# Optimization experiments

Measured on AMD Instinct MI355X. Metric: run time of the kernel, lower is better.

## Reference

```python
import jax, jax.numpy as jnp
import numpy as np

B, S, D = 16, 4096, 128
LN_EPS = 1e-5
REC_EPS = 1e-8


def setup_inputs() -> dict:
    key = jax.random.key(0)
    k1, k2, k3, k4 = jax.random.split(key, 4)
    return {
        "C": jax.random.normal(k1, (B, S, D), dtype=jnp.float32),
        "V": jax.random.normal(k2, (B, S, D), dtype=jnp.float32),
        "W": jax.random.normal(k3, (B, S, D), dtype=jnp.float32),
        "encoder_context": jax.random.normal(k4, (B, D), dtype=jnp.float32),
        "time_modulation": jnp.full((1, 1, D), 0.5, dtype=jnp.float32),
        "context_modulation": jnp.full((1, D), 0.5, dtype=jnp.float32),
        "ln_weight": jnp.ones((D,), dtype=jnp.float32),
        "ln_bias": jnp.zeros((D,), dtype=jnp.float32),
    }


def reference(C, V, W, encoder_context, time_modulation, context_modulation, ln_weight, ln_bias):
    b_, s_, d_ = C.shape
    tm = time_modulation[0, 0]  # [D]
    # context gate is time-invariant: compute once
    ctx_add = jax.nn.sigmoid(encoder_context * context_modulation) * encoder_context  # [B,D]

    def step(carry, xs):
        a, bst = carry  # a: [B,1], bst: [B,D]
        c_t, v_t, w_t = xs  # each [B,D]
        decay = jax.nn.sigmoid(w_t * tm)  # [B,D]
        ec = jnp.exp(c_t)  # [B,D]
        a = decay.mean(axis=1, keepdims=True) * a + ec.sum(axis=1, keepdims=True)
        bst = decay * bst + ec * v_t + ctx_add
        out_t = bst / (a + REC_EPS)
        return (a, bst), out_t

    a0 = jnp.zeros((b_, 1), dtype=C.dtype)
    b0 = jnp.zeros((b_, d_), dtype=C.dtype)
    xs = (jnp.swapaxes(C, 0, 1), jnp.swapaxes(V, 0, 1), jnp.swapaxes(W, 0, 1))  # [S,B,D]
    _, ys = jax.lax.scan(step, (a0, b0), xs)  # ys: [S,B,D]
    res = jnp.swapaxes(ys, 0, 1)  # [B,S,D]

    mu = jnp.mean(res, axis=-1, keepdims=True)
    var = jnp.var(res, axis=-1, keepdims=True)
    normed = (res - mu) * jax.lax.rsqrt(var + LN_EPS)
    return normed * ln_weight + ln_bias
```

## Files before the change

### kernel.cpp

```cpp
#include <hip/hip_runtime.h>

#define BB   16
#define SS   4096
#define DD   128
#define NCH  512
#define TT   (SS / NCH)
#define WPB  4
#define NTHR 256
#define NWAVE (BB * NCH)

#define LN_EPS  1e-5f
#define REC_EPS 1e-8f

__device__ __forceinline__ float fast_rcp(float x) { return __builtin_amdgcn_rcpf(x); }
__device__ __forceinline__ float sigm(float x) { return fast_rcp(1.0f + __expf(-x)); }

template<int CTRL>
__device__ __forceinline__ float dpp_mov0(float x) {
    return __int_as_float(
        __builtin_amdgcn_update_dpp(0, __float_as_int(x), CTRL, 0xF, 0xF, true));
}

__device__ __forceinline__ void wave_red2(float& a, float& b) {
    a += dpp_mov0<0x111>(a); b += dpp_mov0<0x111>(b);
    a += dpp_mov0<0x112>(a); b += dpp_mov0<0x112>(b);
    a += dpp_mov0<0x114>(a); b += dpp_mov0<0x114>(b);
    a += dpp_mov0<0x118>(a); b += dpp_mov0<0x118>(b);
    a += dpp_mov0<0x142>(a); b += dpp_mov0<0x142>(b);
    a += dpp_mov0<0x143>(a); b += dpp_mov0<0x143>(b);
    a = __int_as_float(__builtin_amdgcn_readlane(__float_as_int(a), 63));
    b = __int_as_float(__builtin_amdgcn_readlane(__float_as_int(b), 63));
}

typedef const __attribute__((address_space(1))) unsigned int gas_u32;
typedef __attribute__((address_space(3))) unsigned int las_u32;
__device__ __forceinline__ void gload_lds16(const void* g, void* l) {
    __builtin_amdgcn_global_load_lds((gas_u32*)g, (las_u32*)l, 16, 0, 0);
}
#define VM_WAIT() asm volatile("s_waitcnt vmcnt(0)" ::: "memory")

__global__ __launch_bounds__(NTHR, 3) void pass1_kernel(
    const float* __restrict__ C, const float* __restrict__ V, const float* __restrict__ W,
    const float* __restrict__ enc, const float* __restrict__ tmod, const float* __restrict__ cmod,
    float2* __restrict__ PQ,
    float2* __restrict__ PaQa)
{
    __shared__ float lds[WPB][3][TT * DD];

    const int wv   = threadIdx.x >> 6;
    const int lane = threadIdx.x & 63;
    const int gc   = blockIdx.x * WPB + wv;
    const int b    = gc >> 9;
    const int ch   = gc & (NCH - 1);
    const int d2   = lane << 1;

    const int t0 = ch * TT;
    const size_t chunk = ((size_t)b * SS + t0) * DD;
    const char* Cc = (const char*)(C + chunk);
    const char* Wc = (const char*)(W + chunk);
    const char* Vc = (const char*)(V + chunk);

#pragma unroll
    for (int i = 0; i < 4; ++i) {
        const size_t bo = (size_t)i * 1024 + (size_t)lane * 16;
        gload_lds16(Cc + bo, &lds[wv][0][i * 256]);
        gload_lds16(Wc + bo, &lds[wv][1][i * 256]);
        gload_lds16(Vc + bo, &lds[wv][2][i * 256]);
    }

    const float2 tm = *(const float2*)(tmod + d2);
    const float2 cm = *(const float2*)(cmod + d2);
    const float2 ec = *(const float2*)(enc + b * DD + d2);

    VM_WAIT();

    float2 ctx;
    ctx.x = sigm(ec.x * cm.x) * ec.x;
    ctx.y = sigm(ec.y * cm.y) * ec.y;

    float2 P = make_float2(1.f, 1.f);
    float2 Q = make_float2(0.f, 0.f);
    float sdp[TT], sep[TT];

#pragma unroll
    for (int t = 0; t < TT; ++t) {
        const float2 cv = *(const float2*)&lds[wv][0][t * DD + d2];
        const float2 wl = *(const float2*)&lds[wv][1][t * DD + d2];
        const float2 vl = *(const float2*)&lds[wv][2][t * DD + d2];

        float2 dec, e2, T2;
        dec.x = sigm(wl.x * tm.x); dec.y = sigm(wl.y * tm.y);
        e2.x = __expf(cv.x); e2.y = __expf(cv.y);
        T2.x = e2.x * vl.x + ctx.x;
        T2.y = e2.y * vl.y + ctx.y;

        Q.x = dec.x * Q.x + T2.x;
        Q.y = dec.y * Q.y + T2.y;
        P.x *= dec.x; P.y *= dec.y;

        sdp[t] = dec.x + dec.y;
        sep[t] = e2.x + e2.y;
    }

#pragma unroll
    for (int t = 0; t < TT; ++t) wave_red2(sdp[t], sep[t]);

    float pa = 1.f, qa = 0.f;
#pragma unroll
    for (int t = 0; t < TT; ++t) {
        const float mt = sdp[t] * (1.0f / DD);
        pa *= mt;
        qa = mt * qa + sep[t];
    }

    float4 pq4;
    pq4.x = P.x; pq4.y = Q.x; pq4.z = P.y; pq4.w = Q.y;
    *(float4*)(PQ + (size_t)gc * DD + d2) = pq4;
    if (lane == 0) PaQa[gc] = make_float2(pa, qa);
}

__global__ __launch_bounds__(256, 4) void pass2_kernel(
    const float2* __restrict__ PQ, const float2* __restrict__ PaQa,
    float* __restrict__ bst0,
    float* __restrict__ a0)
{
    const int wv   = threadIdx.x >> 6;
    const int lane = threadIdx.x & 63;
    const int wid  = blockIdx.x * 4 + wv;

    if (wid < BB * DD) {
        const int b = wid >> 7;
        const int d = wid & (DD - 1);
        const int ch0 = lane * 8;
        const size_t base = ((size_t)b * NCH + ch0) * DD + d;

        float2 A[8];
#pragma unroll
        for (int i = 0; i < 8; ++i) A[i] = PQ[base + (size_t)i * DD];

        float p = 1.f, q = 0.f;
#pragma unroll
        for (int i = 0; i < 8; ++i) { q = A[i].x * q + A[i].y; p = A[i].x * p; }

#pragma unroll
        for (int dl = 1; dl < 64; dl <<= 1) {
            float ps = __shfl_up(p, dl);
            float qs = __shfl_up(q, dl);
            ps = (lane >= dl) ? ps : 1.f;
            qs = (lane >= dl) ? qs : 0.f;
            q = p * qs + q;
            p = p * ps;
        }

        float x = __shfl_up(q, 1);
        x = (lane >= 1) ? x : 0.f;

#pragma unroll
        for (int i = 0; i < 8; ++i) {
            bst0[base + (size_t)i * DD] = x;
            x = A[i].x * x + A[i].y;
        }
    } else if (wid < BB * DD + BB) {
        const int b = wid - BB * DD;
        const int ch0 = lane * 8;

        float2 A[8];
#pragma unroll
        for (int i = 0; i < 8; ++i) A[i] = PaQa[b * NCH + ch0 + i];

        float p = 1.f, q = 0.f;
#pragma unroll
        for (int i = 0; i < 8; ++i) { q = A[i].x * q + A[i].y; p = A[i].x * p; }

#pragma unroll
        for (int dl = 1; dl < 64; dl <<= 1) {
            float ps = __shfl_up(p, dl);
            float qs = __shfl_up(q, dl);
            ps = (lane >= dl) ? ps : 1.f;
            qs = (lane >= dl) ? qs : 0.f;
            q = p * qs + q;
            p = p * ps;
        }

        float x = __shfl_up(q, 1);
        x = (lane >= 1) ? x : 0.f;
#pragma unroll
        for (int i = 0; i < 8; ++i) {
            a0[b * NCH + ch0 + i] = x;
            x = A[i].x * x + A[i].y;
        }
    }
}

__global__ __launch_bounds__(NTHR, 3) void pass3_kernel(
    const float* __restrict__ C, const float* __restrict__ V, const float* __restrict__ W,
    const float* __restrict__ enc, const float* __restrict__ tmod, const float* __restrict__ cmod,
    const float* __restrict__ lnw, const float* __restrict__ lnb,
    const float* __restrict__ bst0, const float* __restrict__ a0,
    float* __restrict__ out)
{
    __shared__ float lds[WPB][3][TT * DD];

    const int wv   = threadIdx.x >> 6;
    const int lane = threadIdx.x & 63;
    const int gc   = blockIdx.x * WPB + wv;
    const int b    = gc >> 9;
    const int ch   = gc & (NCH - 1);
    const int d2   = lane << 1;

    const int t0 = ch * TT;
    const size_t chunk = ((size_t)b * SS + t0) * DD;
    const char* Cc = (const char*)(C + chunk);
    const char* Wc = (const char*)(W + chunk);
    const char* Vc = (const char*)(V + chunk);
    float2* Op = (float2*)(out + chunk + d2);

#pragma unroll
    for (int i = 0; i < 4; ++i) {
        const size_t bo = (size_t)i * 1024 + (size_t)lane * 16;
        gload_lds16(Cc + bo, &lds[wv][0][i * 256]);
        gload_lds16(Wc + bo, &lds[wv][1][i * 256]);
        gload_lds16(Vc + bo, &lds[wv][2][i * 256]);
    }

    const float2 tm = *(const float2*)(tmod + d2);
    const float2 cm = *(const float2*)(cmod + d2);
    const float2 ec = *(const float2*)(enc + b * DD + d2);
    const float2 gw = *(const float2*)(lnw + d2);
    const float2 gb = *(const float2*)(lnb + d2);
    float2 bst = *(const float2*)(bst0 + (size_t)gc * DD + d2);
    const float a_in = a0[gc];

    VM_WAIT();

    float2 ctx;
    ctx.x = sigm(ec.x * cm.x) * ec.x;
    ctx.y = sigm(ec.y * cm.y) * ec.y;

    float sdp[TT], sep[TT];
#pragma unroll
    for (int t = 0; t < TT; ++t) {
        const float2 cv = *(const float2*)&lds[wv][0][t * DD + d2];
        const float2 wl = *(const float2*)&lds[wv][1][t * DD + d2];
        sdp[t] = sigm(wl.x * tm.x) + sigm(wl.y * tm.y);
        sep[t] = __expf(cv.x) + __expf(cv.y);
    }
#pragma unroll
    for (int t = 0; t < TT; ++t) wave_red2(sdp[t], sep[t]);

    float a = a_in;
    float2 o[TT];
    float s1p[TT], s2p[TT];
#pragma unroll
    for (int t = 0; t < TT; ++t) {
        const float2 cv = *(const float2*)&lds[wv][0][t * DD + d2];
        const float2 wl = *(const float2*)&lds[wv][1][t * DD + d2];
        const float2 vl = *(const float2*)&lds[wv][2][t * DD + d2];

        float2 dec, e2, T2;
        dec.x = sigm(wl.x * tm.x); dec.y = sigm(wl.y * tm.y);
        e2.x = __expf(cv.x); e2.y = __expf(cv.y);
        T2.x = e2.x * vl.x + ctx.x;
        T2.y = e2.y * vl.y + ctx.y;

        const float mt = sdp[t] * (1.0f / DD);
        a = mt * a + sep[t];
        bst.x = dec.x * bst.x + T2.x;
        bst.y = dec.y * bst.y + T2.y;

        const float inva = fast_rcp(a + REC_EPS);
        o[t].x = bst.x * inva; o[t].y = bst.y * inva;
        s1p[t] = o[t].x + o[t].y;
        s2p[t] = o[t].x * o[t].x + o[t].y * o[t].y;
    }

#pragma unroll
    for (int t = 0; t < TT; ++t) wave_red2(s1p[t], s2p[t]);

#pragma unroll
    for (int t = 0; t < TT; ++t) {
        const float mu  = s1p[t] * (1.0f / DD);
        const float var = s2p[t] * (1.0f / DD) - mu * mu;
        const float rs  = rsqrtf(var + LN_EPS);
        float2 r;
        r.x = (o[t].x - mu) * rs * gw.x + gb.x;
        r.y = (o[t].y - mu) * rs * gw.y + gb.y;
        Op[t * (DD / 2)] = r;
    }
}

extern "C" void kernel_launch(void* const* d_in, const int* in_sizes, int n_in,
                              void* d_out, int out_size, void* d_ws, size_t ws_size,
                              hipStream_t stream)
{
    const float* C    = (const float*)d_in[0];
    const float* V    = (const float*)d_in[1];
    const float* W    = (const float*)d_in[2];
    const float* enc  = (const float*)d_in[3];
    const float* tmod = (const float*)d_in[4];
    const float* cmod = (const float*)d_in[5];
    const float* lnw  = (const float*)d_in[6];
    const float* lnb  = (const float*)d_in[7];
    float* out = (float*)d_out;

    float2* PQ   = (float2*)d_ws;
    float2* PaQa = PQ + (size_t)NWAVE * DD;
    float*  bst0 = (float*)(PaQa + NWAVE);
    float*  a0   = bst0 + (size_t)NWAVE * DD;

    const int nblk = NWAVE / WPB;
    pass1_kernel<<<nblk, NTHR, 0, stream>>>(C, V, W, enc, tmod, cmod, PQ, PaQa);
    pass2_kernel<<<(BB * DD + BB) / 4, 256, 0, stream>>>(PQ, PaQa, bst0, a0);
    pass3_kernel<<<nblk, NTHR, 0, stream>>>(C, V, W, enc, tmod, cmod, lnw, lnb,
                                            bst0, a0, out);
}
```

Baseline: 167.7 us.

## Process eight chunks per wave with double-buffered LDS prefetch in passes 1 and 3

Passes 1 and 3 now have each wave walk eight consecutive time chunks instead of one. C, W and V tiles are streamed into a two-slot LDS ring with global_load_lds, using explicit vmcnt waits so the next chunk's loads overlap the current chunk's compute. Blocks shrink to two waves and the grid shrinks eightfold, which cuts the number of resident waves per CU. Latency hiding now depends on the software pipeline rather than on wave-level parallelism.

Result: slower. 179.8 us (+7.2%).

```diff
diff --git a/kernel.cpp b/kernel.cpp
--- a/kernel.cpp
+++ b/kernel.cpp
@@ -5,9 +5,10 @@
 #define DD   128
 #define NCH  512
 #define TT   (SS / NCH)
-#define WPB  4
-#define NTHR 256
 #define NWAVE (BB * NCH)
+#define KCH  8
+#define P13_WPB 2
+#define P13_NBLK (NWAVE / KCH / P13_WPB)
 
 #define LN_EPS  1e-5f
 #define REC_EPS 1e-8f
@@ -37,92 +38,113 @@
 __device__ __forceinline__ void gload_lds16(const void* g, void* l) {
     __builtin_amdgcn_global_load_lds((gas_u32*)g, (las_u32*)l, 16, 0, 0);
 }
-#define VM_WAIT() asm volatile("s_waitcnt vmcnt(0)" ::: "memory")
-
-__global__ __launch_bounds__(NTHR, 3) void pass1_kernel(
+
+#define VMWAIT(n) asm volatile("s_waitcnt vmcnt(" #n ")" ::: "memory")
+#define LGKWAIT() asm volatile("s_waitcnt lgkmcnt(0)" ::: "memory")
+
+__global__ __launch_bounds__(128, 1) void pass1_kernel(
     const float* __restrict__ C, const float* __restrict__ V, const float* __restrict__ W,
     const float* __restrict__ enc, const float* __restrict__ tmod, const float* __restrict__ cmod,
     float2* __restrict__ PQ,
     float2* __restrict__ PaQa)
 {
-    __shared__ float lds[WPB][3][TT * DD];
+    __shared__ __align__(16) float lds[P13_WPB][2][3][TT * DD];
 
     const int wv   = threadIdx.x >> 6;
     const int lane = threadIdx.x & 63;
-    const int gc   = blockIdx.x * WPB + wv;
-    const int b    = gc >> 9;
-    const int ch   = gc & (NCH - 1);
+    const int wid  = blockIdx.x * P13_WPB + wv;
+    const int gc0  = wid * KCH;
+    const int b    = gc0 >> 9;
+    const int ch0  = gc0 & (NCH - 1);
     const int d2   = lane << 1;
 
-    const int t0 = ch * TT;
-    const size_t chunk = ((size_t)b * SS + t0) * DD;
-    const char* Cc = (const char*)(C + chunk);
-    const char* Wc = (const char*)(W + chunk);
-    const char* Vc = (const char*)(V + chunk);
-
-#pragma unroll
-    for (int i = 0; i < 4; ++i) {
-        const size_t bo = (size_t)i * 1024 + (size_t)lane * 16;
-        gload_lds16(Cc + bo, &lds[wv][0][i * 256]);
-        gload_lds16(Wc + bo, &lds[wv][1][i * 256]);
-        gload_lds16(Vc + bo, &lds[wv][2][i * 256]);
-    }
+    const size_t chunk0 = ((size_t)b * SS + ch0 * TT) * DD;
+    const char* Cc = (const char*)(C + chunk0);
+    const char* Wc = (const char*)(W + chunk0);
+    const char* Vc = (const char*)(V + chunk0);
+
+#define P1_ISSUE(k) do { \
+    LGKWAIT(); \
+    const char* Cb_ = Cc + (size_t)(k) * 4096 + (size_t)lane * 16; \
+    const char* Wb_ = Wc + (size_t)(k) * 4096 + (size_t)lane * 16; \
+    const char* Vb_ = Vc + (size_t)(k) * 4096 + (size_t)lane * 16; \
+    _Pragma("unroll") \
+    for (int i = 0; i < 4; ++i) { \
+        gload_lds16(Cb_ + i * 1024, &lds[wv][(k) & 1][0][i * 256]); \
+        gload_lds16(Wb_ + i * 1024, &lds[wv][(k) & 1][1][i * 256]); \
+        gload_lds16(Vb_ + i * 1024, &lds[wv][(k) & 1][2][i * 256]); \
+    } \
+} while (0)
+
+    P1_ISSUE(0);
+    P1_ISSUE(1);
 
     const float2 tm = *(const float2*)(tmod + d2);
     const float2 cm = *(const float2*)(cmod + d2);
     const float2 ec = *(const float2*)(enc + b * DD + d2);
-
-    VM_WAIT();
-
     float2 ctx;
     ctx.x = sigm(ec.x * cm.x) * ec.x;
     ctx.y = sigm(ec.y * cm.y) * ec.y;
 
-    float2 P = make_float2(1.f, 1.f);
-    float2 Q = make_float2(0.f, 0.f);
-    float sdp[TT], sep[TT];
-
-#pragma unroll
-    for (int t = 0; t < TT; ++t) {
-        const float2 cv = *(const float2*)&lds[wv][0][t * DD + d2];
-        const float2 wl = *(const float2*)&lds[wv][1][t * DD + d2];
-        const float2 vl = *(const float2*)&lds[wv][2][t * DD + d2];
-
-        float2 dec, e2, T2;
-        dec.x = sigm(wl.x * tm.x); dec.y = sigm(wl.y * tm.y);
-        e2.x = __expf(cv.x); e2.y = __expf(cv.y);
-        T2.x = e2.x * vl.x + ctx.x;
-        T2.y = e2.y * vl.y + ctx.y;
-
-        Q.x = dec.x * Q.x + T2.x;
-        Q.y = dec.y * Q.y + T2.y;
-        P.x *= dec.x; P.y *= dec.y;
-
-        sdp[t] = dec.x + dec.y;
-        sep[t] = e2.x + e2.y;
+    float2 Pr[KCH], Qr[KCH];
+    float paR[KCH], qaR[KCH];
+
+#define P1_CH(k) do { \
+    float2 P = make_float2(1.f, 1.f), Q = make_float2(0.f, 0.f); \
+    float sdp[TT], sep[TT]; \
+    _Pragma("unroll") \
+    for (int t = 0; t < TT; ++t) { \
+        const float2 cv = *(const float2*)&lds[wv][(k) & 1][0][t * DD + d2]; \
+        const float2 wl = *(const float2*)&lds[wv][(k) & 1][1][t * DD + d2]; \
+        const float2 vl = *(const float2*)&lds[wv][(k) & 1][2][t * DD + d2]; \
+        float2 dec, e2, T2; \
+        dec.x = sigm(wl.x * tm.x); dec.y = sigm(wl.y * tm.y); \
+        e2.x = __expf(cv.x); e2.y = __expf(cv.y); \
+        T2.x = e2.x * vl.x + ctx.x; \
+        T2.y = e2.y * vl.y + ctx.y; \
+        Q.x = dec.x * Q.x + T2.x; \
+        Q.y = dec.y * Q.y + T2.y; \
+        P.x *= dec.x; P.y *= dec.y; \
+        sdp[t] = dec.x + dec.y; sep[t] = e2.x + e2.y; \
+    } \
+    _Pragma("unroll") \
+    for (int t = 0; t < TT; ++t) wave_red2(sdp[t], sep[t]); \
+    float pa = 1.f, qa = 0.f; \
+    _Pragma("unroll") \
+    for (int t = 0; t < TT; ++t) { \
+        const float mt = sdp[t] * (1.0f / DD); \
+        pa *= mt; qa = mt * qa + sep[t]; \
+    } \
+    Pr[k] = P; Qr[k] = Q; paR[k] = pa; qaR[k] = qa; \
+} while (0)
+
+    VMWAIT(12); P1_CH(0); P1_ISSUE(2);
+    VMWAIT(12); P1_CH(1); P1_ISSUE(3);
+    VMWAIT(12); P1_CH(2); P1_ISSUE(4);
+    VMWAIT(12); P1_CH(3); P1_ISSUE(5);
+    VMWAIT(12); P1_CH(4); P1_ISSUE(6);
+    VMWAIT(12); P1_CH(5); P1_ISSUE(7);
+    VMWAIT(12); P1_CH(6);
+    VMWAIT(0);  P1_CH(7);
+
+#undef P1_ISSUE
+#undef P1_CH
+
+#pragma unroll
+    for (int k = 0; k < KCH; ++k) {
+        float4 pq4;
+        pq4.x = Pr[k].x; pq4.y = Qr[k].x; pq4.z = Pr[k].y; pq4.w = Qr[k].y;
+        *(float4*)(PQ + (size_t)(gc0 + k) * DD + d2) = pq4;
     }
-
-#pragma unroll
-    for (int t = 0; t < TT; ++t) wave_red2(sdp[t], sep[t]);
-
-    float pa = 1.f, qa = 0.f;
-#pragma unroll
-    for (int t = 0; t < TT; ++t) {
-        const float mt = sdp[t] * (1.0f / DD);
-        pa *= mt;
-        qa = mt * qa + sep[t];
+    if (lane == 0) {
+#pragma unroll
+        for (int k = 0; k < KCH; ++k) PaQa[gc0 + k] = make_float2(paR[k], qaR[k]);
     }
-
-    float4 pq4;
-    pq4.x = P.x; pq4.y = Q.x; pq4.z = P.y; pq4.w = Q.y;
-    *(float4*)(PQ + (size_t)gc * DD + d2) = pq4;
-    if (lane == 0) PaQa[gc] = make_float2(pa, qa);
 }
 
 __global__ __launch_bounds__(256, 4) void pass2_kernel(
     const float2* __restrict__ PQ, const float2* __restrict__ PaQa,
-    float* __restrict__ bst0,
-    float* __restrict__ a0)
+    float* __restrict__ bst0, float* __restrict__ a0)
 {
     const int wv   = threadIdx.x >> 6;
     const int lane = threadIdx.x & 63;
@@ -154,7 +176,6 @@
 
         float x = __shfl_up(q, 1);
         x = (lane >= 1) ? x : 0.f;
-
 #pragma unroll
         for (int i = 0; i < 8; ++i) {
             bst0[base + (size_t)i * DD] = x;
@@ -192,101 +213,119 @@
     }
 }
 
-__global__ __launch_bounds__(NTHR, 3) void pass3_kernel(
+__global__ __launch_bounds__(128, 1) void pass3_kernel(
     const float* __restrict__ C, const float* __restrict__ V, const float* __restrict__ W,
     const float* __restrict__ enc, const float* __restrict__ tmod, const float* __restrict__ cmod,
     const float* __restrict__ lnw, const float* __restrict__ lnb,
     const float* __restrict__ bst0, const float* __restrict__ a0,
     float* __restrict__ out)
 {
-    __shared__ float lds[WPB][3][TT * DD];
+    __shared__ __align__(16) float lds[P13_WPB][2][3][TT * DD];
 
     const int wv   = threadIdx.x >> 6;
     const int lane = threadIdx.x & 63;
-    const int gc   = blockIdx.x * WPB + wv;
-    const int b    = gc >> 9;
-    const int ch   = gc & (NCH - 1);
+    const int wid  = blockIdx.x * P13_WPB + wv;
+    const int gc0  = wid * KCH;
+    const int b    = gc0 >> 9;
+    const int ch0  = gc0 & (NCH - 1);
     const int d2   = lane << 1;
 
-    const int t0 = ch * TT;
-    const size_t chunk = ((size_t)b * SS + t0) * DD;
-    const char* Cc = (const char*)(C + chunk);
-    const char* Wc = (const char*)(W + chunk);
-    const char* Vc = (const char*)(V + chunk);
-    float2* Op = (float2*)(out + chunk + d2);
-
-#pragma unroll
-    for (int i = 0; i < 4; ++i) {
-        const size_t bo = (size_t)i * 1024 + (size_t)lane * 16;
-        gload_lds16(Cc + bo, &lds[wv][0][i * 256]);
-        gload_lds16(Wc + bo, &lds[wv][1][i * 256]);
-        gload_lds16(Vc + bo, &lds[wv][2][i * 256]);
+    const size_t chunk0 = ((size_t)b * SS + ch0 * TT) * DD;
+    const char* Cc = (const char*)(C + chunk0);
+    const char* Wc = (const char*)(W + chunk0);
+    const char* Vc = (const char*)(V + chunk0);
+
+    float2 bstR[KCH]; float a0R[KCH];
+#pragma unroll
+    for (int k = 0; k < KCH; ++k) {
+        bstR[k] = *(const float2*)(bst0 + (size_t)(gc0 + k) * DD + d2);
+        a0R[k]  = a0[gc0 + k];
     }
-
     const float2 tm = *(const float2*)(tmod + d2);
     const float2 cm = *(const float2*)(cmod + d2);
     const float2 ec = *(const float2*)(enc + b * DD + d2);
     const float2 gw = *(const float2*)(lnw + d2);
     const float2 gb = *(const float2*)(lnb + d2);
-    float2 bst = *(const float2*)(bst0 + (size_t)gc * DD + d2);
-    const float a_in = a0[gc];
-
-    VM_WAIT();
+
+#define P3_ISSUE(k) do { \
+    LGKWAIT(); \
+    const char* Cb_ = Cc + (size_t)(k) * 4096 + (size_t)lane * 16; \
+    const char* Wb_ = Wc + (size_t)(k) * 4096 + (size_t)lane * 16; \
+    const char* Vb_ = Vc + (size_t)(k) * 4096 + (size_t)lane * 16; \
+    _Pragma("unroll") \
+    for (int i = 0; i < 4; ++i) { \
+        gload_lds16(Cb_ + i * 1024, &lds[wv][(k) & 1][0][i * 256]); \
+        gload_lds16(Wb_ + i * 1024, &lds[wv][(k) & 1][1][i * 256]); \
+        gload_lds16(Vb_ + i * 1024, &lds[wv][(k) & 1][2][i * 256]); \
+    } \
+} while (0)
+
+    P3_ISSUE(0);
+    P3_ISSUE(1);
 
     float2 ctx;
     ctx.x = sigm(ec.x * cm.x) * ec.x;
     ctx.y = sigm(ec.y * cm.y) * ec.y;
 
-    float sdp[TT], sep[TT];
-#pragma unroll
-    for (int t = 0; t < TT; ++t) {
-        const float2 cv = *(const float2*)&lds[wv][0][t * DD + d2];
-        const float2 wl = *(const float2*)&lds[wv][1][t * DD + d2];
-        sdp[t] = sigm(wl.x * tm.x) + sigm(wl.y * tm.y);
-        sep[t] = __expf(cv.x) + __expf(cv.y);
-    }
-#pragma unroll
-    for (int t = 0; t < TT; ++t) wave_red2(sdp[t], sep[t]);
-
-    float a = a_in;
-    float2 o[TT];
-    float s1p[TT], s2p[TT];
-#pragma unroll
-    for (int t = 0; t < TT; ++t) {
-        const float2 cv = *(const float2*)&lds[wv][0][t * DD + d2];
-        const float2 wl = *(const float2*)&lds[wv][1][t * DD + d2];
-        const float2 vl = *(const float2*)&lds[wv][2][t * DD + d2];
-
-        float2 dec, e2, T2;
-        dec.x = sigm(wl.x * tm.x); dec.y = sigm(wl.y * tm.y);
-        e2.x = __expf(cv.x); e2.y = __expf(cv.y);
-        T2.x = e2.x * vl.x + ctx.x;
-        T2.y = e2.y * vl.y + ctx.y;
-
-        const float mt = sdp[t] * (1.0f / DD);
-        a = mt * a + sep[t];
-        bst.x = dec.x * bst.x + T2.x;
-        bst.y = dec.y * bst.y + T2.y;
-
-        const float inva = fast_rcp(a + REC_EPS);
-        o[t].x = bst.x * inva; o[t].y = bst.y * inva;
-        s1p[t] = o[t].x + o[t].y;
-        s2p[t] = o[t].x * o[t].x + o[t].y * o[t].y;
-    }
-
-#pragma unroll
-    for (int t = 0; t < TT; ++t) wave_red2(s1p[t], s2p[t]);
-
-#pragma unroll
-    for (int t = 0; t < TT; ++t) {
-        const float mu  = s1p[t] * (1.0f / DD);
-        const float var = s2p[t] * (1.0f / DD) - mu * mu;
-        const float rs  = rsqrtf(var + LN_EPS);
-        float2 r;
-        r.x = (o[t].x - mu) * rs * gw.x + gb.x;
-        r.y = (o[t].y - mu) * rs * gw.y + gb.y;
-        Op[t * (DD / 2)] = r;
-    }
+#define P3_CH(k) do { \
+    float sdp[TT], sep[TT]; \
+    _Pragma("unroll") \
+    for (int t = 0; t < TT; ++t) { \
+        const float2 cv = *(const float2*)&lds[wv][(k) & 1][0][t * DD + d2]; \
+        const float2 wl = *(const float2*)&lds[wv][(k) & 1][1][t * DD + d2]; \
+        sdp[t] = sigm(wl.x * tm.x) + sigm(wl.y * tm.y); \
+        sep[t] = __expf(cv.x) + __expf(cv.y); \
+    } \
+    _Pragma("unroll") \
+    for (int t = 0; t < TT; ++t) wave_red2(sdp[t], sep[t]); \
+    float a = a0R[k]; \
+    float2 bst = bstR[k]; \
+    float2 o[TT]; float s1p[TT], s2p[TT]; \
+    _Pragma("unroll") \
+    for (int t = 0; t < TT; ++t) { \
+        const float2 cv = *(const float2*)&lds[wv][(k) & 1][0][t * DD + d2]; \
+        const float2 wl = *(const float2*)&lds[wv][(k) & 1][1][t * DD + d2]; \
+        const float2 vl = *(const float2*)&lds[wv][(k) & 1][2][t * DD + d2]; \
+        float2 dec, e2, T2; \
+        dec.x = sigm(wl.x * tm.x); dec.y = sigm(wl.y * tm.y); \
+        e2.x = __expf(cv.x); e2.y = __expf(cv.y); \
+        T2.x = e2.x * vl.x + ctx.x; \
+        T2.y = e2.y * vl.y + ctx.y; \
+        const float mt = sdp[t] * (1.0f / DD); \
+        a = mt * a + sep[t]; \
+        bst.x = dec.x * bst.x + T2.x; \
+        bst.y = dec.y * bst.y + T2.y; \
+        const float inva = fast_rcp(a + REC_EPS); \
+        o[t].x = bst.x * inva; o[t].y = bst.y * inva; \
+        s1p[t] = o[t].x + o[t].y; \
+        s2p[t] = o[t].x * o[t].x + o[t].y * o[t].y; \
+    } \
+    _Pragma("unroll") \
+    for (int t = 0; t < TT; ++t) wave_red2(s1p[t], s2p[t]); \
+    float2* Op = (float2*)(out + chunk0 + (size_t)(k) * TT * DD + d2); \
+    _Pragma("unroll") \
+    for (int t = 0; t < TT; ++t) { \
+        const float mu  = s1p[t] * (1.0f / DD); \
+        const float var = s2p[t] * (1.0f / DD) - mu * mu; \
+        const float rs  = rsqrtf(var + LN_EPS); \
+        float2 r; \
+        r.x = (o[t].x - mu) * rs * gw.x + gb.x; \
+        r.y = (o[t].y - mu) * rs * gw.y + gb.y; \
+        Op[t * (DD / 2)] = r; \
+    } \
+} while (0)
+
+    VMWAIT(12); P3_CH(0); P3_ISSUE(2);
+    VMWAIT(12); P3_CH(1); P3_ISSUE(3);
+    VMWAIT(12); P3_CH(2); P3_ISSUE(4);
+    VMWAIT(12); P3_CH(3); P3_ISSUE(5);
+    VMWAIT(12); P3_CH(4); P3_ISSUE(6);
+    VMWAIT(12); P3_CH(5); P3_ISSUE(7);
+    VMWAIT(12); P3_CH(6);
+    VMWAIT(8);  P3_CH(7);
+
+#undef P3_ISSUE
+#undef P3_CH
 }
 
 extern "C" void kernel_launch(void* const* d_in, const int* in_sizes, int n_in,
@@ -308,9 +347,8 @@
     float*  bst0 = (float*)(PaQa + NWAVE);
     float*  a0   = bst0 + (size_t)NWAVE * DD;
 
-    const int nblk = NWAVE / WPB;
-    pass1_kernel<<<nblk, NTHR, 0, stream>>>(C, V, W, enc, tmod, cmod, PQ, PaQa);
+    pass1_kernel<<<P13_NBLK, 128, 0, stream>>>(C, V, W, enc, tmod, cmod, PQ, PaQa);
     pass2_kernel<<<(BB * DD + BB) / 4, 256, 0, stream>>>(PQ, PaQa, bst0, a0);
-    pass3_kernel<<<nblk, NTHR, 0, stream>>>(C, V, W, enc, tmod, cmod, lnw, lnb,
-                                            bst0, a0, out);
-}
+    pass3_kernel<<<P13_NBLK, 128, 0, stream>>>(C, V, W, enc, tmod, cmod, lnw, lnb,
+                                               bst0, a0, out);
+}
```
